# Optimization experiments

Hardware: AMD Instinct MI355X
Metric: run time of the kernel (lower is better)

The kernel has to match this reference:

```python
import jax, jax.numpy as jnp
import numpy as np

B, N, D, C, S = 128, 100000, 256, 2000, 751  # batch, memory size, feat dim, num classes, source classes
TEMP = 0.05
EPS = 1e-06


def _l2norm(x):
    return x / jnp.linalg.norm(x, axis=-1, keepdims=True)


def setup_inputs() -> dict:
    key = jax.random.key(0)
    k1, k2, k3, k4, k5 = jax.random.split(key, 5)
    inputs = _l2norm(jax.random.normal(k1, (B, D), dtype=jnp.float32))
    inputs2 = _l2norm(jax.random.normal(k2, (B, D), dtype=jnp.float32))
    features = _l2norm(jax.random.normal(k3, (N, D), dtype=jnp.float32))
    labels = jax.random.randint(k4, (N,), 0, C)
    labels = labels.at[:C].set(jnp.arange(C))  # ensure labels.max()+1 == C
    indexes = jax.random.randint(k5, (B,), 0, N)
    return {"inputs": inputs, "inputs2": inputs2, "features": features,
            "labels": labels, "indexes": indexes, "source_classes": S}


def reference(inputs, inputs2, features, labels, indexes, source_classes):
    # memory-bank logits, [B, N]
    logits = (inputs @ features.T) / TEMP
    logits2 = (inputs2 @ features.T) / TEMP
    targets = labels[indexes]  # [B]

    # per-class counts and segment-mean of logits over the bank, [C, B]
    nums = jax.ops.segment_sum(jnp.ones((N,), jnp.float32), labels, num_segments=C)  # [C]
    denom = jnp.where(nums > 0, nums, 1.0)[:, None]  # [C, 1]
    sim = jax.ops.segment_sum(logits.T, labels, num_segments=C) / denom   # [C, B]
    sim2 = jax.ops.segment_sum(logits2.T, labels, num_segments=C) / denom  # [C, B]

    # MSE between class-probability maps over the first source_classes classes
    p1 = sim[:source_classes].T   # [B, S]
    p2 = sim2[:source_classes].T  # [B, S]
    diff = jax.nn.softmax(p1, axis=1) - jax.nn.softmax(p2, axis=1)
    loss_mse = jnp.sum(diff * diff) / source_classes

    # hard-positive/negative mining: per-class max of logits (0 for empty classes)
    seg_max = jax.ops.segment_max(logits.T, labels, num_segments=C)  # [C, B], -inf where empty
    present = (nums > 0)  # [C]
    sim_hard = jnp.where(present[:, None], seg_max, 0.0).T  # [B, C]
    # for the target class, use the hardest (min) positive instead
    seg_min = jax.ops.segment_min(logits.T, labels, num_segments=C)  # [C, B]
    b_idx = jnp.arange(B)
    sim_hard = sim_hard.at[b_idx, targets].set(seg_min[targets, b_idx])

    # masked softmax over present classes + NLL
    mask = present.astype(jnp.float32)[None, :]  # [1, C]
    exps = jnp.exp(sim_hard) * mask
    masked_sim = exps / (jnp.sum(exps, axis=1, keepdims=True) + EPS)
    loss_con = -jnp.mean(jnp.log(masked_sim[b_idx, targets] + EPS))

    return (loss_con, loss_mse)
```

## Files before the change

### kernel.cpp

```cpp
#include <hip/hip_runtime.h>
#include <hip/hip_bf16.h>

#define BB 128
#define NN 100000
#define DD 256
#define CC 2000
#define SS 751
#define INVTEMP 20.0f
#define EPSV 1e-6f

#define HIST_BLOCKS 391
#define PREP_BLOCKS 32
#define NTILES_MAX 3563

typedef __attribute__((ext_vector_type(8))) short bf16x8;
typedef __attribute__((ext_vector_type(8))) unsigned short u16x8;
typedef __attribute__((ext_vector_type(4))) float f32x4;

__device__ __forceinline__ unsigned short f2bf(float x) {
    unsigned int u = __float_as_uint(x);
    u += 0x7fffu + ((u >> 16) & 1u);
    return (unsigned short)(u >> 16);
}

__device__ __forceinline__ u16x8 cvt8u(float4 a, float4 b) {
    union { unsigned u[4]; u16x8 v; } cv;
    asm("v_cvt_pk_bf16_f32 %0, %1, %2" : "=v"(cv.u[0]) : "v"(a.x), "v"(a.y));
    asm("v_cvt_pk_bf16_f32 %0, %1, %2" : "=v"(cv.u[1]) : "v"(a.z), "v"(a.w));
    asm("v_cvt_pk_bf16_f32 %0, %1, %2" : "=v"(cv.u[2]) : "v"(b.x), "v"(b.y));
    asm("v_cvt_pk_bf16_f32 %0, %1, %2" : "=v"(cv.u[3]) : "v"(b.z), "v"(b.w));
    return cv.v;
}

__global__ __launch_bounds__(256) void hist_prep_kernel(
    const int* __restrict__ labels, int* __restrict__ counts,
    const float* __restrict__ in1, const float* __restrict__ in2,
    unsigned short* __restrict__ inb)
{
    int bid = blockIdx.x;
    if (bid < HIST_BLOCKS) {
        int n = bid * 256 + threadIdx.x;
        if (n < NN) atomicAdd(&counts[labels[n]], 1);
    } else {
        int ch = (bid - HIST_BLOCKS) * 256 + threadIdx.x;
        if (ch >= 8192) return;
        int l  = ch & 63;
        int kc = (ch >> 6) & 7;
        int nr = ch >> 9;
        int row = nr * 16 + (l & 15);
        const float* src = (row < BB) ? (in1 + (size_t)row * DD)
                                      : (in2 + (size_t)(row - BB) * DD);
        int k0 = kc * 32 + ((l >> 4) << 3);
        u16x8 o;
        #pragma unroll
        for (int j = 0; j < 8; ++j) o[j] = f2bf(src[k0 + j]);
        *(u16x8*)(inb + (size_t)ch * 8) = o;
    }
}

__global__ __launch_bounds__(256) void scan_kernel(const int* __restrict__ counts,
                                                   int* __restrict__ tile_start,
                                                   int* __restrict__ cursor,
                                                   int* __restrict__ tile_meta,
                                                   int* __restrict__ ntiles_total,
                                                   float* __restrict__ out) {
    const int PT = 8;
    int tid = threadIdx.x;
    if (tid == 0) { out[0] = 0.f; out[1] = 0.f; }
    int tcnt[PT];
    int tot = 0;
    #pragma unroll
    for (int i = 0; i < PT; ++i) {
        int c = tid * PT + i;
        tcnt[i] = (c < CC) ? ((counts[c] + 63) >> 6) : 0;
        tot += tcnt[i];
    }
    __shared__ int sh[256];
    sh[tid] = tot;
    __syncthreads();
    for (int ofs = 1; ofs < 256; ofs <<= 1) {
        int v = (tid >= ofs) ? sh[tid - ofs] : 0;
        __syncthreads();
        sh[tid] += v;
        __syncthreads();
    }
    if (tid == 255) *ntiles_total = sh[255];
    int run = sh[tid] - tot;
    #pragma unroll
    for (int i = 0; i < PT; ++i) {
        int c = tid * PT + i;
        if (c < CC) {
            tile_start[c] = run;
            cursor[c] = run << 6;
            for (int j = 0; j < tcnt[i]; ++j)
                tile_meta[run + j] = (c << 5) | j;
        }
        run += tcnt[i];
    }
}

__global__ void scatter_idx(const int* __restrict__ labels, int* __restrict__ cursor,
                            int* __restrict__ sorted_idx) {
    int n = blockIdx.x * 256 + threadIdx.x;
    if (n < NN) {
        int c = labels[n];
        int p = atomicAdd(&cursor[c], 1);
        sorted_idx[p] = n;
    }
}

__global__ __launch_bounds__(256, 4) void mm_kernel(
    const float* __restrict__ features, const unsigned short* __restrict__ inb,
    const int* __restrict__ sorted_idx, const int* __restrict__ tile_meta,
    const int* __restrict__ counts, const int* __restrict__ ntiles_total,
    float* __restrict__ part_max, float* __restrict__ part_min,
    float* __restrict__ part_sA, float* __restrict__ part_sB)
{
    const int t = blockIdx.x >> 1;
    if (t >= *ntiles_total) return;
    const int rh  = blockIdx.x & 1;
    const int tid = threadIdx.x;
    const int w   = tid >> 6;
    const int l   = tid & 63;
    const int meta = tile_meta[t];
    const int base_local = (meta & 31) << 6;
    const int cnt  = counts[meta >> 5];
    const int vrows = cnt - base_local;

    __shared__ __align__(16) char ldsA[16384];

    {
        const int m0 = tid >> 3;
        const int g  = tid & 7;
        const int rowg = rh * 32 + m0;
        if (rowg < vrows) {
            int n = sorted_idx[t * 64 + rowg];
            const float* src = features + (size_t)n * DD;
            const int ma = m0 >> 4;
            #pragma unroll
            for (int s = 0; s < 4; ++s) {
                int k0 = s * 64 + g * 8;
                float4 a = *(const float4*)(src + k0);
                float4 b = *(const float4*)(src + k0 + 4);
                u16x8 o = cvt8u(a, b);
                int crow = s * 8 + g;
                int kc   = crow >> 2;
                int ks   = crow & 3;
                int cch  = (ks << 4) | ((m0 & 15) ^ kc);
                *(u16x8*)(&ldsA[0] + (((ma * 8 + kc) << 10) | (cch << 4))) = o;
            }
        }
    }
    __syncthreads();

    f32x4 acc[2][4];
    #pragma unroll
    for (int ma = 0; ma < 2; ++ma)
        #pragma unroll
        for (int nb = 0; nb < 4; ++nb)
            acc[ma][nb] = (f32x4){0.f, 0.f, 0.f, 0.f};

    __builtin_amdgcn_s_setprio(1);
    #pragma unroll
    for (int kc = 0; kc < 8; ++kc) {
        bf16x8 b[4];
        #pragma unroll
        for (int nb = 0; nb < 4; ++nb)
            b[nb] = *(const bf16x8*)(inb + (((size_t)((4 * w + nb) * 8 + kc) * 64 + l) << 3));
        int lx = (l ^ kc) << 4;
        #pragma unroll
        for (int ma = 0; ma < 2; ++ma) {
            bf16x8 a = *(const bf16x8*)(&ldsA[0] + ((ma * 8 + kc) << 10) + lx);
            #pragma unroll
            for (int nb = 0; nb < 4; ++nb)
                acc[ma][nb] = __builtin_amdgcn_mfma_f32_16x16x32_bf16(a, b[nb], acc[ma][nb], 0, 0, 0);
        }
    }
    __builtin_amdgcn_s_setprio(0);

    const int h4 = (l >> 4) << 2;
    const bool do_mm = (w < 2);
    float sm[4] = {0.f, 0.f, 0.f, 0.f};
    float mx[4] = {-3.4e38f, -3.4e38f, -3.4e38f, -3.4e38f};
    float mn[4] = { 3.4e38f,  3.4e38f,  3.4e38f,  3.4e38f};
    #pragma unroll
    for (int ma = 0; ma < 2; ++ma) {
        #pragma unroll
        for (int reg = 0; reg < 4; ++reg) {
            bool valid = (rh * 32 + 16 * ma + h4 + reg) < vrows;
            if (valid) {
                #pragma unroll
                for (int nb = 0; nb < 4; ++nb) {
                    float v = acc[ma][nb][reg];
                    sm[nb] += v;
                    if (do_mm) {
                        mx[nb] = fmaxf(mx[nb], v);
                        mn[nb] = fminf(mn[nb], v);
                    }
                }
            }
        }
    }
    #pragma unroll
    for (int nb = 0; nb < 4; ++nb) {
        sm[nb] += __shfl_xor(sm[nb], 16);
        sm[nb] += __shfl_xor(sm[nb], 32);
        if (do_mm) {
            mx[nb] = fmaxf(mx[nb], __shfl_xor(mx[nb], 16));
            mx[nb] = fmaxf(mx[nb], __shfl_xor(mx[nb], 32));
            mn[nb] = fminf(mn[nb], __shfl_xor(mn[nb], 16));
            mn[nb] = fminf(mn[nb], __shfl_xor(mn[nb], 32));
        }
    }
    if (l < 16) {
        #pragma unroll
        for (int nb = 0; nb < 4; ++nb) {
            int col = 64 * (w & 1) + 16 * nb + l;
            size_t p = (size_t)(2 * t + rh) * 128 + col;
            if (do_mm) { part_max[p] = mx[nb]; part_min[p] = mn[nb]; part_sA[p] = sm[nb]; }
            else       { part_sB[p] = sm[nb]; }
        }
    }
}


__device__ __forceinline__ float blk_reduce_sum(float v) {
    __shared__ float sh[4];
    int lane = threadIdx.x & 63, w = threadIdx.x >> 6;
    #pragma unroll
    for (int o = 32; o; o >>= 1) v += __shfl_down(v, o, 64);
    __syncthreads();
    if (lane == 0) sh[w] = v;
    __syncthreads();
    return sh[0] + sh[1] + sh[2] + sh[3];
}

__device__ __forceinline__ float blk_reduce_max(float v) {
    __shared__ float sh[4];
    int lane = threadIdx.x & 63, w = threadIdx.x >> 6;
    #pragma unroll
    for (int o = 32; o; o >>= 1) v = fmaxf(v, __shfl_down(v, o, 64));
    __syncthreads();
    if (lane == 0) sh[w] = v;
    __syncthreads();
    return fmaxf(fmaxf(sh[0], sh[1]), fmaxf(sh[2], sh[3]));
}

__global__ __launch_bounds__(256) void finalize_kernel(
    const float* __restrict__ part_max, const float* __restrict__ part_min,
    const float* __restrict__ part_sA, const float* __restrict__ part_sB,
    const int* __restrict__ tile_start, const int* __restrict__ counts,
    const int* __restrict__ labels, const int* __restrict__ indexes,
    float* __restrict__ out)
{
    const int b   = blockIdx.x;
    const int tid = threadIdx.x;
    const int tgt = labels[indexes[b]];

    __shared__ float a1[SS], a2[SS];
    __shared__ float sh_etgt;

    float local = 0.f;
    for (int c = tid; c < CC; c += 256) {
        int cnt = counts[c];
        if (cnt > 0) {
            int st0 = tile_start[c] * 2;
            int nst = ((cnt + 63) >> 6) * 2;
            bool src = (c < SS);
            float mx = -3.4e38f, sA = 0.f, sB = 0.f;
            for (int j = 0; j < nst; ++j) {
                size_t p = (size_t)(st0 + j) * 128 + b;
                mx = fmaxf(mx, part_max[p]);
                if (src) { sA += part_sA[p]; sB += part_sB[p]; }
            }
            float v = mx;
            if (c == tgt) {
                float mn = 3.4e38f;
                for (int j = 0; j < nst; ++j)
                    mn = fminf(mn, part_min[(size_t)(st0 + j) * 128 + b]);
                v = mn;
            }
            float e = expf(v * INVTEMP);
            local += e;
            if (c == tgt) sh_etgt = e;
            if (src) {
                float icnt = INVTEMP / (float)cnt;
                a1[c] = sA * icnt;
                a2[c] = sB * icnt;
            }
        } else if (c < SS) {
            a1[c] = 0.f;
            a2[c] = 0.f;
        }
    }
    float sum_e = blk_reduce_sum(local);
    float etgt = sh_etgt;
    float loss_con_b = -logf(etgt / (sum_e + EPSV) + EPSV);

    float m1 = -3.4e38f, m2 = -3.4e38f;
    for (int c = tid; c < SS; c += 256) { m1 = fmaxf(m1, a1[c]); m2 = fmaxf(m2, a2[c]); }
    m1 = blk_reduce_max(m1);
    m2 = blk_reduce_max(m2);
    float s1 = 0.f, s2 = 0.f;
    for (int c = tid; c < SS; c += 256) { s1 += expf(a1[c] - m1); s2 += expf(a2[c] - m2); }
    s1 = blk_reduce_sum(s1);
    s2 = blk_reduce_sum(s2);
    float inv1 = 1.f / s1, inv2 = 1.f / s2;
    float dsum = 0.f;
    for (int c = tid; c < SS; c += 256) {
        float d = expf(a1[c] - m1) * inv1 - expf(a2[c] - m2) * inv2;
        dsum += d * d;
    }
    dsum = blk_reduce_sum(dsum);
    if (tid == 0) {
        atomicAdd(&out[0], loss_con_b * (1.0f / (float)BB));
        atomicAdd(&out[1], dsum * (1.0f / (float)SS));
    }
}


extern "C" void kernel_launch(void* const* d_in, const int* in_sizes, int n_in,
                              void* d_out, int out_size, void* d_ws, size_t ws_size,
                              hipStream_t stream) {
    const float* inputs   = (const float*)d_in[0];
    const float* inputs2  = (const float*)d_in[1];
    const float* features = (const float*)d_in[2];
    const int*   labels   = (const int*)d_in[3];
    const int*   indexes  = (const int*)d_in[4];

    float* out = (float*)d_out;

    int* wsi = (int*)d_ws;
    int* counts     = wsi;
    int* tile_start = wsi + 2048;
    int* cursor     = wsi + 4096;
    int* ntiles     = wsi + 6144;
    unsigned short* inb = (unsigned short*)(wsi + 6160);
    int* tile_meta  = wsi + 38928;
    int* sorted_idx = wsi + 42496;
    float* part_max = (float*)(wsi + 270592);
    float* part_min = part_max + (size_t)NTILES_MAX * 256;
    float* part_sA  = part_min + (size_t)NTILES_MAX * 256;
    float* part_sB  = part_sA  + (size_t)NTILES_MAX * 256;

    hipMemsetAsync(counts, 0, 2048 * sizeof(int), stream);

    hist_prep_kernel<<<HIST_BLOCKS + PREP_BLOCKS, 256, 0, stream>>>(
        labels, counts, inputs, inputs2, inb);
    scan_kernel<<<1, 256, 0, stream>>>(counts, tile_start, cursor, tile_meta, ntiles, out);
    scatter_idx<<<HIST_BLOCKS, 256, 0, stream>>>(labels, cursor, sorted_idx);
    mm_kernel<<<2 * NTILES_MAX, 256, 0, stream>>>(features, inb, sorted_idx, tile_meta,
                                                  counts, ntiles,
                                                  part_max, part_min, part_sA, part_sB);
    finalize_kernel<<<BB, 256, 0, stream>>>(part_max, part_min, part_sA, part_sB,
                                            tile_start, counts, labels, indexes, out);
}
```

Baseline: 100.5 us.

## Double mm_kernel block to 512 threads and prefetch B fragments before LDS staging

```diff
diff --git a/kernel.cpp b/kernel.cpp
--- a/kernel.cpp
+++ b/kernel.cpp
@@ -109,7 +109,7 @@
     }
 }
 
-__global__ __launch_bounds__(256, 4) void mm_kernel(
+__global__ __launch_bounds__(512, 4) void mm_kernel(
     const float* __restrict__ features, const unsigned short* __restrict__ inb,
     const int* __restrict__ sorted_idx, const int* __restrict__ tile_meta,
     const int* __restrict__ counts, const int* __restrict__ ntiles_total,
@@ -129,60 +129,64 @@
 
     __shared__ __align__(16) char ldsA[16384];
 
+    bf16x8 bfr[16];
+    #pragma unroll
+    for (int kc = 0; kc < 8; ++kc)
+        #pragma unroll
+        for (int nb = 0; nb < 2; ++nb)
+            bfr[kc * 2 + nb] = *(const bf16x8*)(inb + (((size_t)((2 * w + nb) * 8 + kc) * 64 + l) << 3));
+
     {
-        const int m0 = tid >> 3;
-        const int g  = tid & 7;
+        const int m0 = tid >> 4;
+        const int g  = tid & 15;
         const int rowg = rh * 32 + m0;
         if (rowg < vrows) {
             int n = sorted_idx[t * 64 + rowg];
-            const float* src = features + (size_t)n * DD;
+            const float* src = features + (size_t)n * DD + g * 16;
+            float4 a0 = *(const float4*)(src);
+            float4 a1 = *(const float4*)(src + 4);
+            float4 b0 = *(const float4*)(src + 8);
+            float4 b1 = *(const float4*)(src + 12);
+            u16x8 o0 = cvt8u(a0, a1);
+            u16x8 o1 = cvt8u(b0, b1);
             const int ma = m0 >> 4;
             #pragma unroll
-            for (int s = 0; s < 4; ++s) {
-                int k0 = s * 64 + g * 8;
-                float4 a = *(const float4*)(src + k0);
-                float4 b = *(const float4*)(src + k0 + 4);
-                u16x8 o = cvt8u(a, b);
-                int crow = s * 8 + g;
+            for (int h = 0; h < 2; ++h) {
+                int crow = 2 * g + h;
                 int kc   = crow >> 2;
                 int ks   = crow & 3;
                 int cch  = (ks << 4) | ((m0 & 15) ^ kc);
-                *(u16x8*)(&ldsA[0] + (((ma * 8 + kc) << 10) | (cch << 4))) = o;
-            }
-        }
-    }
-    __syncthreads();
-
-    f32x4 acc[2][4];
+                *(u16x8*)(&ldsA[0] + (((ma * 8 + kc) << 10) | (cch << 4))) = (h == 0) ? o0 : o1;
+            }
+        }
+    }
+    __syncthreads();
+
+    f32x4 acc[2][2];
     #pragma unroll
     for (int ma = 0; ma < 2; ++ma)
         #pragma unroll
-        for (int nb = 0; nb < 4; ++nb)
+        for (int nb = 0; nb < 2; ++nb)
             acc[ma][nb] = (f32x4){0.f, 0.f, 0.f, 0.f};
 
     __builtin_amdgcn_s_setprio(1);
     #pragma unroll
     for (int kc = 0; kc < 8; ++kc) {
-        bf16x8 b[4];
-        #pragma unroll
-        for (int nb = 0; nb < 4; ++nb)
-            b[nb] = *(const bf16x8*)(inb + (((size_t)((4 * w + nb) * 8 + kc) * 64 + l) << 3));
         int lx = (l ^ kc) << 4;
         #pragma unroll
         for (int ma = 0; ma < 2; ++ma) {
             bf16x8 a = *(const bf16x8*)(&ldsA[0] + ((ma * 8 + kc) << 10) + lx);
-            #pragma unroll
-            for (int nb = 0; nb < 4; ++nb)
-                acc[ma][nb] = __builtin_amdgcn_mfma_f32_16x16x32_bf16(a, b[nb], acc[ma][nb], 0, 0, 0);
+            acc[ma][0] = __builtin_amdgcn_mfma_f32_16x16x32_bf16(a, bfr[kc * 2 + 0], acc[ma][0], 0, 0, 0);
+            acc[ma][1] = __builtin_amdgcn_mfma_f32_16x16x32_bf16(a, bfr[kc * 2 + 1], acc[ma][1], 0, 0, 0);
         }
     }
     __builtin_amdgcn_s_setprio(0);
 
     const int h4 = (l >> 4) << 2;
-    const bool do_mm = (w < 2);
-    float sm[4] = {0.f, 0.f, 0.f, 0.f};
-    float mx[4] = {-3.4e38f, -3.4e38f, -3.4e38f, -3.4e38f};
-    float mn[4] = { 3.4e38f,  3.4e38f,  3.4e38f,  3.4e38f};
+    const bool do_mm = (w < 4);
+    float sm[2] = {0.f, 0.f};
+    float mx[2] = {-3.4e38f, -3.4e38f};
+    float mn[2] = { 3.4e38f,  3.4e38f};
     #pragma unroll
     for (int ma = 0; ma < 2; ++ma) {
         #pragma unroll
@@ -190,7 +194,7 @@
             bool valid = (rh * 32 + 16 * ma + h4 + reg) < vrows;
             if (valid) {
                 #pragma unroll
-                for (int nb = 0; nb < 4; ++nb) {
+                for (int nb = 0; nb < 2; ++nb) {
                     float v = acc[ma][nb][reg];
                     sm[nb] += v;
                     if (do_mm) {
@@ -202,7 +206,7 @@
         }
     }
     #pragma unroll
-    for (int nb = 0; nb < 4; ++nb) {
+    for (int nb = 0; nb < 2; ++nb) {
         sm[nb] += __shfl_xor(sm[nb], 16);
         sm[nb] += __shfl_xor(sm[nb], 32);
         if (do_mm) {
@@ -214,8 +218,8 @@
     }
     if (l < 16) {
         #pragma unroll
-        for (int nb = 0; nb < 4; ++nb) {
-            int col = 64 * (w & 1) + 16 * nb + l;
+        for (int nb = 0; nb < 2; ++nb) {
+            int col = 32 * (w & 3) + 16 * nb + l;
             size_t p = (size_t)(2 * t + rh) * 128 + col;
             if (do_mm) { part_max[p] = mx[nb]; part_min[p] = mn[nb]; part_sA[p] = sm[nb]; }
             else       { part_sB[p] = sm[nb]; }
@@ -349,7 +353,7 @@
         labels, counts, inputs, inputs2, inb);
     scan_kernel<<<1, 256, 0, stream>>>(counts, tile_start, cursor, tile_meta, ntiles, out);
     scatter_idx<<<HIST_BLOCKS, 256, 0, stream>>>(labels, cursor, sorted_idx);
-    mm_kernel<<<2 * NTILES_MAX, 256, 0, stream>>>(features, inb, sorted_idx, tile_meta,
+    mm_kernel<<<2 * NTILES_MAX, 512, 0, stream>>>(features, inb, sorted_idx, tile_meta,
                                                   counts, ntiles,
                                                   part_max, part_min, part_sA, part_sB);
     finalize_kernel<<<BB, 256, 0, stream>>>(part_max, part_min, part_sA, part_sB,
```

Result: slower. 103.5 us (+3.0%).
